# Performance work log

Hardware: AMD Instinct MI355X
Metric: run time of the kernel (lower is better)

The kernel has to match this reference:

```python
import jax, jax.numpy as jnp
import numpy as np

DEPTH = 3


def _outer(a, b):
    # batched tensor product of flattened tensor-algebra levels: (B, m) x (B, n) -> (B, m*n)
    return (a[:, :, None] * b[:, None, :]).reshape(a.shape[0], -1)


def _signature(X, depth):
    """Truncated path signature via Chen's identity (matches signatory.signature,
    basepoint=False). X: (B, T, C) -> (B, sum_k C^k)."""
    B, T, C = X.shape
    dX = X[:, 1:, :] - X[:, :-1, :]  # (B, T-1, C) increments

    def exp_levels(dx):
        # exp(dx) in truncated tensor algebra: level k = dx^{\otimes k} / k!
        e = [dx]
        for k in range(2, depth + 1):
            e.append(_outer(e[-1], dx) / k)
        return e

    def step(S, dx):
        e = exp_levels(dx)
        new = []
        for k in range(1, depth + 1):
            t = S[k - 1] + e[k - 1]  # terms with S_0=1 or e_0=1
            for i in range(1, k):
                t = t + _outer(S[i - 1], e[k - i - 1])
            new.append(t)
        return tuple(new), None

    init = tuple(jnp.zeros((B, C ** k), X.dtype) for k in range(1, depth + 1))
    S, _ = jax.lax.scan(step, init, jnp.swapaxes(dX, 0, 1))  # scan over time
    return jnp.concatenate(S, axis=1)


def setup_inputs() -> dict:
    key = jax.random.key(0)
    kx, kw, kb = jax.random.split(key, 3)
    B, T, C, n_out = 2048, 128, 8, 10
    sig_dim = sum(C ** k for k in range(1, DEPTH + 1))  # 584
    X = jax.random.normal(kx, (B, T, C), dtype=jnp.float32)
    bound = 1.0 / np.sqrt(sig_dim)
    W = jax.random.uniform(kw, (n_out, sig_dim), jnp.float32, -bound, bound)
    b = jax.random.uniform(kb, (n_out,), jnp.float32, -bound, bound)
    return {"X": X, "W": W, "b": b}


def reference(X, W, b):
    sig = _signature(X, DEPTH)          # (B, sig_dim)
    out = sig @ W.T + b                  # (B, n_outputs)
    return out.reshape(-1, W.shape[0])
```

## Files before the change

kernel.cpp:

```cpp
#include <hip/hip_runtime.h>

#define B_TOTAL 2048
#define T_LEN 128
#define C_DIM 8
#define NOUT 10
#define SIG_DIM 584
#define WAVES_PER_BLOCK 4

__global__ __launch_bounds__(256) void sig_linear_kernel(
    const float* __restrict__ X, const float* __restrict__ W,
    const float* __restrict__ bias, float* __restrict__ out)
{
    __shared__ __align__(16) float lds[WAVES_PER_BLOCK][T_LEN * C_DIM];
    const int tid = threadIdx.x;
    const int w = tid >> 6;
    const int l = tid & 63;
    const int b = blockIdx.x * WAVES_PER_BLOCK + w;
    const int i = l >> 3;
    const int j = l & 7;

    const float4* Xb4 = reinterpret_cast<const float4*>(X + (size_t)b * (T_LEN * C_DIM));
    float4* lds4 = reinterpret_cast<float4*>(&lds[w][0]);
#pragma unroll
    for (int r = 0; r < 4; ++r) lds4[r * 64 + l] = Xb4[r * 64 + l];
    __syncthreads();

    const float* L = &lds[w][0];

    float s3[8];
#pragma unroll
    for (int k = 0; k < 8; ++k) s3[k] = 0.f;
    float s2 = 0.f, s1i = 0.f, s1j = 0.f;

    float xp[8];
    {
        float4 r0 = *reinterpret_cast<const float4*>(L);
        float4 r1 = *reinterpret_cast<const float4*>(L + 4);
        xp[0] = r0.x; xp[1] = r0.y; xp[2] = r0.z; xp[3] = r0.w;
        xp[4] = r1.x; xp[5] = r1.y; xp[6] = r1.z; xp[7] = r1.w;
    }
    float xpi = L[i], xpj = L[j];

    for (int t = 1; t < T_LEN; ++t) {
        const float* row = L + t * C_DIM;
        float4 r0 = *reinterpret_cast<const float4*>(row);
        float4 r1 = *reinterpret_cast<const float4*>(row + 4);
        float xc[8];
        xc[0] = r0.x; xc[1] = r0.y; xc[2] = r0.z; xc[3] = r0.w;
        xc[4] = r1.x; xc[5] = r1.y; xc[6] = r1.z; xc[7] = r1.w;
        float xci = row[i], xcj = row[j];

        float dx[8];
#pragma unroll
        for (int k = 0; k < 8; ++k) { dx[k] = xc[k] - xp[k]; xp[k] = xc[k]; }
        float dxi = xci - xpi, dxj = xcj - xpj;
        xpi = xci; xpj = xcj;

        float cij = dxi * dxj;
        float f = s2 + 0.5f * s1i * dxj + (1.0f / 6.0f) * cij;
#pragma unroll
        for (int k = 0; k < 8; ++k) s3[k] = fmaf(f, dx[k], s3[k]);
        s2 = fmaf(0.5f, cij, fmaf(s1i, dxj, s2));
        s1i += dxi;
        s1j += dxj;
    }

#pragma unroll
    for (int o = 0; o < NOUT; ++o) {
        const float* wrow = W + o * SIG_DIM;
        float part = s2 * wrow[8 + l];
        const float4 w0 = *reinterpret_cast<const float4*>(wrow + 72 + l * 8);
        const float4 w1 = *reinterpret_cast<const float4*>(wrow + 72 + l * 8 + 4);
        part = fmaf(s3[0], w0.x, part); part = fmaf(s3[1], w0.y, part);
        part = fmaf(s3[2], w0.z, part); part = fmaf(s3[3], w0.w, part);
        part = fmaf(s3[4], w1.x, part); part = fmaf(s3[5], w1.y, part);
        part = fmaf(s3[6], w1.z, part); part = fmaf(s3[7], w1.w, part);
        if (i == 0) part = fmaf(s1j, wrow[j], part);
#pragma unroll
        for (int off = 32; off > 0; off >>= 1) part += __shfl_xor(part, off);
        if (l == 0) out[b * NOUT + o] = part + bias[o];
    }
}

extern "C" void kernel_launch(void* const* d_in, const int* in_sizes, int n_in,
                              void* d_out, int out_size, void* d_ws, size_t ws_size,
                              hipStream_t stream) {
    const float* X = (const float*)d_in[0];
    const float* W = (const float*)d_in[1];
    const float* bias = (const float*)d_in[2];
    float* out = (float*)d_out;
    dim3 grid(B_TOTAL / WAVES_PER_BLOCK);
    dim3 block(64 * WAVES_PER_BLOCK);
    sig_linear_kernel<<<grid, block, 0, stream>>>(X, W, bias, out);
}
```

Baseline: 23.57 us.

## Split each path's time scan across four waves and merge with Chen's identity

Assigns one batch element per block and splits its 127 time steps across four waves, each computing a partial signature over 32 increments. The partial signatures go to LDS and are combined sequentially with Chen's identity, and the output dot products are spread across waves. Increments are precomputed into LDS and broadcast with readlane instead of being recomputed by every lane. This shortens the serial dependency chain per wave and adds parallelism, at the cost of extra LDS traffic, barriers and merge arithmetic.

```diff
diff --git a/kernel.cpp b/kernel.cpp
--- a/kernel.cpp
+++ b/kernel.cpp
@@ -1,72 +1,119 @@
 #include <hip/hip_runtime.h>
 
-#define B_TOTAL 2048
-#define T_LEN 128
-#define C_DIM 8
 #define NOUT 10
 #define SIG_DIM 584
-#define WAVES_PER_BLOCK 4
 
-__global__ __launch_bounds__(256) void sig_linear_kernel(
+__device__ __forceinline__ float rdlane(float x, int lane) {
+    return __int_as_float(__builtin_amdgcn_readlane(__float_as_int(x), lane));
+}
+
+__global__ __launch_bounds__(256, 4) void sig_linear_kernel(
     const float* __restrict__ X, const float* __restrict__ W,
     const float* __restrict__ bias, float* __restrict__ out)
 {
-    __shared__ __align__(16) float lds[WAVES_PER_BLOCK][T_LEN * C_DIM];
+    __shared__ __align__(16) float s_path[1024];
+    __shared__ __align__(16) float s_dx[1024];
+    __shared__ __align__(16) float s_sig[4 * SIG_DIM];
+
     const int tid = threadIdx.x;
     const int w = tid >> 6;
     const int l = tid & 63;
-    const int b = blockIdx.x * WAVES_PER_BLOCK + w;
     const int i = l >> 3;
     const int j = l & 7;
+    const int b = blockIdx.x;
 
-    const float4* Xb4 = reinterpret_cast<const float4*>(X + (size_t)b * (T_LEN * C_DIM));
-    float4* lds4 = reinterpret_cast<float4*>(&lds[w][0]);
-#pragma unroll
-    for (int r = 0; r < 4; ++r) lds4[r * 64 + l] = Xb4[r * 64 + l];
+    const float4* Xb4 = reinterpret_cast<const float4*>(X + (size_t)b * 1024);
+    reinterpret_cast<float4*>(s_path)[tid] = Xb4[tid];
     __syncthreads();
 
-    const float* L = &lds[w][0];
+    const int idx = w * 256 + l * 4;
+    const bool v = idx < 1016;
+    float4 d4;
+    {
+        const float4 a  = *reinterpret_cast<const float4*>(s_path + idx);
+        const float4 c4 = *reinterpret_cast<const float4*>(s_path + (v ? idx + 8 : idx));
+        d4.x = v ? (c4.x - a.x) : 0.f;
+        d4.y = v ? (c4.y - a.y) : 0.f;
+        d4.z = v ? (c4.z - a.z) : 0.f;
+        d4.w = v ? (c4.w - a.w) : 0.f;
+        *reinterpret_cast<float4*>(s_dx + idx) = d4;
+    }
+    __syncthreads();
 
     float s3[8];
 #pragma unroll
     for (int k = 0; k < 8; ++k) s3[k] = 0.f;
     float s2 = 0.f, s1i = 0.f, s1j = 0.f;
 
-    float xp[8];
-    {
-        float4 r0 = *reinterpret_cast<const float4*>(L);
-        float4 r1 = *reinterpret_cast<const float4*>(L + 4);
-        xp[0] = r0.x; xp[1] = r0.y; xp[2] = r0.z; xp[3] = r0.w;
-        xp[4] = r1.x; xp[5] = r1.y; xp[6] = r1.z; xp[7] = r1.w;
-    }
-    float xpi = L[i], xpj = L[j];
-
-    for (int t = 1; t < T_LEN; ++t) {
-        const float* row = L + t * C_DIM;
-        float4 r0 = *reinterpret_cast<const float4*>(row);
-        float4 r1 = *reinterpret_cast<const float4*>(row + 4);
-        float xc[8];
-        xc[0] = r0.x; xc[1] = r0.y; xc[2] = r0.z; xc[3] = r0.w;
-        xc[4] = r1.x; xc[5] = r1.y; xc[6] = r1.z; xc[7] = r1.w;
-        float xci = row[i], xcj = row[j];
-
-        float dx[8];
+    const float* dxb = s_dx + w * 256;
 #pragma unroll
-        for (int k = 0; k < 8; ++k) { dx[k] = xc[k] - xp[k]; xp[k] = xc[k]; }
-        float dxi = xci - xpi, dxj = xcj - xpj;
-        xpi = xci; xpj = xcj;
-
-        float cij = dxi * dxj;
-        float f = s2 + 0.5f * s1i * dxj + (1.0f / 6.0f) * cij;
-#pragma unroll
-        for (int k = 0; k < 8; ++k) s3[k] = fmaf(f, dx[k], s3[k]);
-        s2 = fmaf(0.5f, cij, fmaf(s1i, dxj, s2));
+    for (int s = 0; s < 32; ++s) {
+        const float dxi = dxb[s * 8 + i];
+        const float dxj = dxb[s * 8 + j];
+        const float k0 = rdlane(d4.x, 2 * s);
+        const float k1 = rdlane(d4.y, 2 * s);
+        const float k2 = rdlane(d4.z, 2 * s);
+        const float k3 = rdlane(d4.w, 2 * s);
+        const float k4 = rdlane(d4.x, 2 * s + 1);
+        const float k5 = rdlane(d4.y, 2 * s + 1);
+        const float k6 = rdlane(d4.z, 2 * s + 1);
+        const float k7 = rdlane(d4.w, 2 * s + 1);
+        const float c = dxi * dxj;
+        const float u = s1i * dxj;
+        const float f = fmaf(0.5f, u, fmaf(1.0f / 6.0f, c, s2));
+        s3[0] = fmaf(f, k0, s3[0]);
+        s3[1] = fmaf(f, k1, s3[1]);
+        s3[2] = fmaf(f, k2, s3[2]);
+        s3[3] = fmaf(f, k3, s3[3]);
+        s3[4] = fmaf(f, k4, s3[4]);
+        s3[5] = fmaf(f, k5, s3[5]);
+        s3[6] = fmaf(f, k6, s3[6]);
+        s3[7] = fmaf(f, k7, s3[7]);
+        s2 = fmaf(0.5f, c, s2 + u);
         s1i += dxi;
         s1j += dxj;
     }
 
+    {
+        float* sg = s_sig + w * SIG_DIM;
+        if (i == 0) sg[j] = s1j;
+        sg[8 + l] = s2;
+        *reinterpret_cast<float4*>(sg + 72 + l * 8) =
+            make_float4(s3[0], s3[1], s3[2], s3[3]);
+        *reinterpret_cast<float4*>(sg + 72 + l * 8 + 4) =
+            make_float4(s3[4], s3[5], s3[6], s3[7]);
+    }
+    __syncthreads();
+
 #pragma unroll
-    for (int o = 0; o < NOUT; ++o) {
+    for (int k = 0; k < 8; ++k) s3[k] = 0.f;
+    s2 = 0.f; s1i = 0.f; s1j = 0.f;
+#pragma unroll
+    for (int c = 0; c < 4; ++c) {
+        const float* sg = s_sig + c * SIG_DIM;
+        const float4 b0 = *reinterpret_cast<const float4*>(sg);
+        const float4 b1 = *reinterpret_cast<const float4*>(sg + 4);
+        const float s1bi = sg[i];
+        const float s1bj = sg[j];
+        const float s2b = sg[8 + l];
+        const float4 q0 = *reinterpret_cast<const float4*>(sg + 8 + j * 8);
+        const float4 q1 = *reinterpret_cast<const float4*>(sg + 8 + j * 8 + 4);
+        const float4 t0 = *reinterpret_cast<const float4*>(sg + 72 + l * 8);
+        const float4 t1 = *reinterpret_cast<const float4*>(sg + 72 + l * 8 + 4);
+        s3[0] = fmaf(s2, b0.x, fmaf(s1i, q0.x, s3[0] + t0.x));
+        s3[1] = fmaf(s2, b0.y, fmaf(s1i, q0.y, s3[1] + t0.y));
+        s3[2] = fmaf(s2, b0.z, fmaf(s1i, q0.z, s3[2] + t0.z));
+        s3[3] = fmaf(s2, b0.w, fmaf(s1i, q0.w, s3[3] + t0.w));
+        s3[4] = fmaf(s2, b1.x, fmaf(s1i, q1.x, s3[4] + t1.x));
+        s3[5] = fmaf(s2, b1.y, fmaf(s1i, q1.y, s3[5] + t1.y));
+        s3[6] = fmaf(s2, b1.z, fmaf(s1i, q1.z, s3[6] + t1.z));
+        s3[7] = fmaf(s2, b1.w, fmaf(s1i, q1.w, s3[7] + t1.w));
+        s2 = s2 + fmaf(s1i, s1bj, s2b);
+        s1i += s1bi;
+        s1j += s1bj;
+    }
+
+    for (int o = w; o < NOUT; o += 4) {
         const float* wrow = W + o * SIG_DIM;
         float part = s2 * wrow[8 + l];
         const float4 w0 = *reinterpret_cast<const float4*>(wrow + 72 + l * 8);
@@ -89,7 +136,5 @@
     const float* W = (const float*)d_in[1];
     const float* bias = (const float*)d_in[2];
     float* out = (float*)d_out;
-    dim3 grid(B_TOTAL / WAVES_PER_BLOCK);
-    dim3 block(64 * WAVES_PER_BLOCK);
-    sig_linear_kernel<<<grid, block, 0, stream>>>(X, W, bias, out);
+    sig_linear_kernel<<<dim3(2048), dim3(256), 0, stream>>>(X, W, bias, out);
 }
```

Result: slower. 24.72 us (+4.9%).

## Precompute increments in transposed LDS and broadcast dx via readlane

Applied to the files above, without the earlier changes.

Each lane now computes path increments directly from global memory and stores them time-major per channel in padded LDS. In the time loop the full dx vector comes from scalar readlane broadcasts of register-held increments, and each lane's own i/j increments are read as float4 from the transposed columns. This removes the per-step subtraction and the repeated full-row LDS reads, at the cost of a fully unrolled 127-step loop with many readlane operations and more code.

```diff
diff --git a/kernel.cpp b/kernel.cpp
--- a/kernel.cpp
+++ b/kernel.cpp
@@ -1,69 +1,102 @@
 #include <hip/hip_runtime.h>
 
-#define B_TOTAL 2048
-#define T_LEN 128
-#define C_DIM 8
 #define NOUT 10
 #define SIG_DIM 584
-#define WAVES_PER_BLOCK 4
+#define TPAD 132
+
+__device__ __forceinline__ float rdlane(float x, int lane) {
+    return __int_as_float(__builtin_amdgcn_readlane(__float_as_int(x), lane));
+}
 
 __global__ __launch_bounds__(256) void sig_linear_kernel(
     const float* __restrict__ X, const float* __restrict__ W,
     const float* __restrict__ bias, float* __restrict__ out)
 {
-    __shared__ __align__(16) float lds[WAVES_PER_BLOCK][T_LEN * C_DIM];
+    __shared__ float s_dxT[4][8 * TPAD];
+
     const int tid = threadIdx.x;
     const int w = tid >> 6;
     const int l = tid & 63;
-    const int b = blockIdx.x * WAVES_PER_BLOCK + w;
     const int i = l >> 3;
     const int j = l & 7;
+    const int b = blockIdx.x * 4 + w;
 
-    const float4* Xb4 = reinterpret_cast<const float4*>(X + (size_t)b * (T_LEN * C_DIM));
-    float4* lds4 = reinterpret_cast<float4*>(&lds[w][0]);
-#pragma unroll
-    for (int r = 0; r < 4; ++r) lds4[r * 64 + l] = Xb4[r * 64 + l];
+    const float* Xb = X + (size_t)b * 1024;
+    float* dxT = &s_dxT[w][0];
+    const int cb = (l & 1) * 4;
+    const int rl = l >> 1;
+
+    float4 dA, dB, dC, dD;
+#define PREP(DQ, QQ)                                                          \
+    {                                                                         \
+        const int r = (QQ) * 32 + rl;                                         \
+        const float* xr = Xb + r * 8 + cb;                                    \
+        const float4 a  = *reinterpret_cast<const float4*>(xr);               \
+        const float4 c4 = *reinterpret_cast<const float4*>(xr + (r < 127 ? 8 : 0)); \
+        DQ.x = (r < 127) ? c4.x - a.x : 0.f;                                  \
+        DQ.y = (r < 127) ? c4.y - a.y : 0.f;                                  \
+        DQ.z = (r < 127) ? c4.z - a.z : 0.f;                                  \
+        DQ.w = (r < 127) ? c4.w - a.w : 0.f;                                  \
+        dxT[(cb + 0) * TPAD + r] = DQ.x;                                      \
+        dxT[(cb + 1) * TPAD + r] = DQ.y;                                      \
+        dxT[(cb + 2) * TPAD + r] = DQ.z;                                      \
+        dxT[(cb + 3) * TPAD + r] = DQ.w;                                      \
+    }
+    PREP(dA, 0) PREP(dB, 1) PREP(dC, 2) PREP(dD, 3)
+#undef PREP
     __syncthreads();
-
-    const float* L = &lds[w][0];
 
     float s3[8];
 #pragma unroll
     for (int k = 0; k < 8; ++k) s3[k] = 0.f;
     float s2 = 0.f, s1i = 0.f, s1j = 0.f;
 
-    float xp[8];
-    {
-        float4 r0 = *reinterpret_cast<const float4*>(L);
-        float4 r1 = *reinterpret_cast<const float4*>(L + 4);
-        xp[0] = r0.x; xp[1] = r0.y; xp[2] = r0.z; xp[3] = r0.w;
-        xp[4] = r1.x; xp[5] = r1.y; xp[6] = r1.z; xp[7] = r1.w;
+    const float* icol = dxT + i * TPAD;
+    const float* jcol = dxT + j * TPAD;
+
+#define STEP(DQ, LB, DXI, DXJ)                                                \
+    {                                                                         \
+        const float k0 = rdlane(DQ.x, (LB));                                  \
+        const float k1 = rdlane(DQ.y, (LB));                                  \
+        const float k2 = rdlane(DQ.z, (LB));                                  \
+        const float k3 = rdlane(DQ.w, (LB));                                  \
+        const float k4 = rdlane(DQ.x, (LB) + 1);                              \
+        const float k5 = rdlane(DQ.y, (LB) + 1);                              \
+        const float k6 = rdlane(DQ.z, (LB) + 1);                              \
+        const float k7 = rdlane(DQ.w, (LB) + 1);                              \
+        const float cc = (DXI) * (DXJ);                                       \
+        const float uu = s1i * (DXJ);                                         \
+        const float f  = fmaf(0.5f, uu, fmaf(1.0f / 6.0f, cc, s2));           \
+        s3[0] = fmaf(f, k0, s3[0]);                                           \
+        s3[1] = fmaf(f, k1, s3[1]);                                           \
+        s3[2] = fmaf(f, k2, s3[2]);                                           \
+        s3[3] = fmaf(f, k3, s3[3]);                                           \
+        s3[4] = fmaf(f, k4, s3[4]);                                           \
+        s3[5] = fmaf(f, k5, s3[5]);                                           \
+        s3[6] = fmaf(f, k6, s3[6]);                                           \
+        s3[7] = fmaf(f, k7, s3[7]);                                           \
+        s2 = fmaf(0.5f, cc, s2 + uu);                                         \
+        s1i += (DXI);                                                         \
+        s1j += (DXJ);                                                         \
     }
-    float xpi = L[i], xpj = L[j];
 
-    for (int t = 1; t < T_LEN; ++t) {
-        const float* row = L + t * C_DIM;
-        float4 r0 = *reinterpret_cast<const float4*>(row);
-        float4 r1 = *reinterpret_cast<const float4*>(row + 4);
-        float xc[8];
-        xc[0] = r0.x; xc[1] = r0.y; xc[2] = r0.z; xc[3] = r0.w;
-        xc[4] = r1.x; xc[5] = r1.y; xc[6] = r1.z; xc[7] = r1.w;
-        float xci = row[i], xcj = row[j];
-
-        float dx[8];
-#pragma unroll
-        for (int k = 0; k < 8; ++k) { dx[k] = xc[k] - xp[k]; xp[k] = xc[k]; }
-        float dxi = xci - xpi, dxj = xcj - xpj;
-        xpi = xci; xpj = xcj;
-
-        float cij = dxi * dxj;
-        float f = s2 + 0.5f * s1i * dxj + (1.0f / 6.0f) * cij;
-#pragma unroll
-        for (int k = 0; k < 8; ++k) s3[k] = fmaf(f, dx[k], s3[k]);
-        s2 = fmaf(0.5f, cij, fmaf(s1i, dxj, s2));
-        s1i += dxi;
-        s1j += dxj;
+#define SECTION(DQ, QQ)                                                       \
+    for (int g = 0; g < 8; ++g) {                                             \
+        const int t0 = (QQ) * 32 + g * 4;                                     \
+        const float4 ic = *reinterpret_cast<const float4*>(icol + t0);        \
+        const float4 jc = *reinterpret_cast<const float4*>(jcol + t0);        \
+        const int lb = g * 8;                                                 \
+        STEP(DQ, lb + 0, ic.x, jc.x)                                          \
+        STEP(DQ, lb + 2, ic.y, jc.y)                                          \
+        STEP(DQ, lb + 4, ic.z, jc.z)                                          \
+        STEP(DQ, lb + 6, ic.w, jc.w)                                          \
     }
+    SECTION(dA, 0)
+    SECTION(dB, 1)
+    SECTION(dC, 2)
+    SECTION(dD, 3)
+#undef SECTION
+#undef STEP
 
 #pragma unroll
     for (int o = 0; o < NOUT; ++o) {
@@ -89,7 +122,5 @@
     const float* W = (const float*)d_in[1];
     const float* bias = (const float*)d_in[2];
     float* out = (float*)d_out;
-    dim3 grid(B_TOTAL / WAVES_PER_BLOCK);
-    dim3 block(64 * WAVES_PER_BLOCK);
-    sig_linear_kernel<<<grid, block, 0, stream>>>(X, W, bias, out);
+    sig_linear_kernel<<<dim3(512), dim3(256), 0, stream>>>(X, W, bias, out);
 }
```

Result: faster. 21.60 us (-8.4%).

## Split each path's time scan across four waves using algebraic level-3 decomposition

Applied to the files above, without the earlier changes.

Instead of one wave scanning all 127 steps for one batch element, each block now handles one element and each of its four waves covers a 32-step time chunk. The level-3 signature is rewritten algebraically so that chunks add independently: the S2 sums are combined through LDS and the X_T term is applied once in the epilogue. Per-step row broadcasts use readlane from registers instead of LDS reads, and a transposed LDS layout serves the i/j columns. This shortens the serial dependency chain by about four times, at the cost of more blocks, extra syncs and a cross-wave reduction of partial outputs.

```diff
diff --git a/kernel.cpp b/kernel.cpp
--- a/kernel.cpp
+++ b/kernel.cpp
@@ -1,85 +1,144 @@
 #include <hip/hip_runtime.h>
 
-#define B_TOTAL 2048
-#define T_LEN 128
-#define C_DIM 8
 #define NOUT 10
 #define SIG_DIM 584
-#define WAVES_PER_BLOCK 4
+#define TS 36
+
+__device__ __forceinline__ float rdlane(float x, int lane) {
+    return __int_as_float(__builtin_amdgcn_readlane(__float_as_int(x), lane));
+}
+__device__ __forceinline__ float comp4(float4 v, int c) {
+    return c == 0 ? v.x : c == 1 ? v.y : c == 2 ? v.z : v.w;
+}
 
 __global__ __launch_bounds__(256) void sig_linear_kernel(
     const float* __restrict__ X, const float* __restrict__ W,
     const float* __restrict__ bias, float* __restrict__ out)
 {
-    __shared__ __align__(16) float lds[WAVES_PER_BLOCK][T_LEN * C_DIM];
+    __shared__ __align__(16) float s_xT[4][8 * TS];
+    __shared__ float s_s2[4][64];
+    __shared__ float s_part[4][16];
+
     const int tid = threadIdx.x;
-    const int w = tid >> 6;
-    const int l = tid & 63;
-    const int b = blockIdx.x * WAVES_PER_BLOCK + w;
-    const int i = l >> 3;
-    const int j = l & 7;
+    const int w = tid >> 6, l = tid & 63, i = l >> 3, j = l & 7;
+    const int b = blockIdx.x;
+    const int t0 = w * 32;
+    const float* Xb = X + (size_t)b * 1024;
 
-    const float4* Xb4 = reinterpret_cast<const float4*>(X + (size_t)b * (T_LEN * C_DIM));
-    float4* lds4 = reinterpret_cast<float4*>(&lds[w][0]);
-#pragma unroll
-    for (int r = 0; r < 4; ++r) lds4[r * 64 + l] = Xb4[r * 64 + l];
+    const int rl_ = l >> 1, cb = (l & 1) * 4;
+    const float4 d4 = *reinterpret_cast<const float4*>(Xb + (t0 + rl_) * 8 + cb);
+    float* xT = &s_xT[w][0];
+    xT[(cb + 0) * TS + rl_] = d4.x;
+    xT[(cb + 1) * TS + rl_] = d4.y;
+    xT[(cb + 2) * TS + rl_] = d4.z;
+    xT[(cb + 3) * TS + rl_] = d4.w;
+    if (l < 2) {
+        const int rN = (t0 + 32 < 128) ? t0 + 32 : 127;
+        const float4 e4 = *reinterpret_cast<const float4*>(Xb + rN * 8 + l * 4);
+        xT[(l * 4 + 0) * TS + 32] = e4.x;
+        xT[(l * 4 + 1) * TS + 32] = e4.y;
+        xT[(l * 4 + 2) * TS + 32] = e4.z;
+        xT[(l * 4 + 3) * TS + 32] = e4.w;
+    }
+    const float x0i = Xb[i];
+    const float x0j = Xb[j];
+    const float s1jv = Xb[1016 + j] - x0j;
     __syncthreads();
 
-    const float* L = &lds[w][0];
+    float A[8];
+#pragma unroll
+    for (int k = 0; k < 8; ++k) A[k] = 0.f;
+    float S2f = 0.f;
 
-    float s3[8];
+    const float* icol = xT + i * TS;
+    const float* jcol = xT + j * TS;
+
+    float xcr[8], xnr[8];
 #pragma unroll
-    for (int k = 0; k < 8; ++k) s3[k] = 0.f;
-    float s2 = 0.f, s1i = 0.f, s1j = 0.f;
+    for (int k = 0; k < 8; ++k)
+        xcr[k] = rdlane(comp4(d4, k & 3), k >> 2);
 
-    float xp[8];
-    {
-        float4 r0 = *reinterpret_cast<const float4*>(L);
-        float4 r1 = *reinterpret_cast<const float4*>(L + 4);
-        xp[0] = r0.x; xp[1] = r0.y; xp[2] = r0.z; xp[3] = r0.w;
-        xp[4] = r1.x; xp[5] = r1.y; xp[6] = r1.z; xp[7] = r1.w;
-    }
-    float xpi = L[i], xpj = L[j];
+    float4 ic = *reinterpret_cast<const float4*>(icol);
+    float4 jc = *reinterpret_cast<const float4*>(jcol);
 
-    for (int t = 1; t < T_LEN; ++t) {
-        const float* row = L + t * C_DIM;
-        float4 r0 = *reinterpret_cast<const float4*>(row);
-        float4 r1 = *reinterpret_cast<const float4*>(row + 4);
-        float xc[8];
-        xc[0] = r0.x; xc[1] = r0.y; xc[2] = r0.z; xc[3] = r0.w;
-        xc[4] = r1.x; xc[5] = r1.y; xc[6] = r1.z; xc[7] = r1.w;
-        float xci = row[i], xcj = row[j];
-
-        float dx[8];
 #pragma unroll
-        for (int k = 0; k < 8; ++k) { dx[k] = xc[k] - xp[k]; xp[k] = xc[k]; }
-        float dxi = xci - xpi, dxj = xcj - xpj;
-        xpi = xci; xpj = xcj;
-
-        float cij = dxi * dxj;
-        float f = s2 + 0.5f * s1i * dxj + (1.0f / 6.0f) * cij;
+    for (int g4 = 0; g4 < 8; ++g4) {
+        float4 in4, jn4;
+        if (g4 < 7) {
+            in4 = *reinterpret_cast<const float4*>(icol + 4 * g4 + 4);
+            jn4 = *reinterpret_cast<const float4*>(jcol + 4 * g4 + 4);
+        } else {
+            in4 = make_float4(icol[32], 0.f, 0.f, 0.f);
+            jn4 = make_float4(jcol[32], 0.f, 0.f, 0.f);
+        }
 #pragma unroll
-        for (int k = 0; k < 8; ++k) s3[k] = fmaf(f, dx[k], s3[k]);
-        s2 = fmaf(0.5f, cij, fmaf(s1i, dxj, s2));
-        s1i += dxi;
-        s1j += dxj;
+        for (int q = 0; q < 4; ++q) {
+            const int s = g4 * 4 + q;
+            const float xci = comp4(ic, q);
+            const float xcj = comp4(jc, q);
+            const float xni = (q < 3) ? comp4(ic, q + 1) : in4.x;
+            const float xnj = (q < 3) ? comp4(jc, q + 1) : jn4.x;
+            if (s < 31) {
+#pragma unroll
+                for (int k = 0; k < 8; ++k)
+                    xnr[k] = rdlane(comp4(d4, k & 3), 2 * (s + 1) + (k >> 2));
+            } else {
+#pragma unroll
+                for (int k = 0; k < 8; ++k) xnr[k] = xT[k * TS + 32];
+            }
+            const float dxi = xni - xci;
+            const float dxj = xnj - xcj;
+            const float cpi = xci - x0i;
+            const float cpj = xcj - x0j;
+            (void)cpj;
+            const float gg = dxj * fmaf(0.5f, dxi, cpi);
+            const float hh = dxj * fmaf(1.0f / 6.0f, dxi, 0.5f * cpi);
+            const float gmh = gg - hh;
+            S2f += gg;
+#pragma unroll
+            for (int k = 0; k < 8; ++k)
+                A[k] = fmaf(gmh, xnr[k], fmaf(hh, xcr[k], A[k]));
+#pragma unroll
+            for (int k = 0; k < 8; ++k) xcr[k] = xnr[k];
+        }
+        ic = in4;
+        jc = jn4;
     }
 
+    s_s2[w][l] = S2f;
+    __syncthreads();
+    const float S2T = s_s2[0][l] + s_s2[1][l] + s_s2[2][l] + s_s2[3][l];
+
+    const float4 x7a = *reinterpret_cast<const float4*>(Xb + 1016);
+    const float4 x7b = *reinterpret_cast<const float4*>(Xb + 1020);
 #pragma unroll
     for (int o = 0; o < NOUT; ++o) {
         const float* wrow = W + o * SIG_DIM;
-        float part = s2 * wrow[8 + l];
         const float4 w0 = *reinterpret_cast<const float4*>(wrow + 72 + l * 8);
         const float4 w1 = *reinterpret_cast<const float4*>(wrow + 72 + l * 8 + 4);
-        part = fmaf(s3[0], w0.x, part); part = fmaf(s3[1], w0.y, part);
-        part = fmaf(s3[2], w0.z, part); part = fmaf(s3[3], w0.w, part);
-        part = fmaf(s3[4], w1.x, part); part = fmaf(s3[5], w1.y, part);
-        part = fmaf(s3[6], w1.z, part); part = fmaf(s3[7], w1.w, part);
-        if (i == 0) part = fmaf(s1j, wrow[j], part);
+        float dA = w0.x * A[0];
+        dA = fmaf(w0.y, A[1], dA); dA = fmaf(w0.z, A[2], dA);
+        dA = fmaf(w0.w, A[3], dA); dA = fmaf(w1.x, A[4], dA);
+        dA = fmaf(w1.y, A[5], dA); dA = fmaf(w1.z, A[6], dA);
+        dA = fmaf(w1.w, A[7], dA);
+        float part = -dA;
+        if (w == 0) {
+            float e = w0.x * x7a.x;
+            e = fmaf(w0.y, x7a.y, e); e = fmaf(w0.z, x7a.z, e);
+            e = fmaf(w0.w, x7a.w, e); e = fmaf(w1.x, x7b.x, e);
+            e = fmaf(w1.y, x7b.y, e); e = fmaf(w1.z, x7b.z, e);
+            e = fmaf(w1.w, x7b.w, e);
+            part = fmaf(S2T, e + wrow[8 + l], part);
+            if (i == 0) part = fmaf(s1jv, wrow[j], part);
+        }
 #pragma unroll
         for (int off = 32; off > 0; off >>= 1) part += __shfl_xor(part, off);
-        if (l == 0) out[b * NOUT + o] = part + bias[o];
+        if (l == o) s_part[w][o] = part;
     }
+    __syncthreads();
+    if (tid < NOUT)
+        out[b * NOUT + tid] = s_part[0][tid] + s_part[1][tid] +
+                              s_part[2][tid] + s_part[3][tid] + bias[tid];
 }
 
 extern "C" void kernel_launch(void* const* d_in, const int* in_sizes, int n_in,
@@ -89,7 +148,5 @@
     const float* W = (const float*)d_in[1];
     const float* bias = (const float*)d_in[2];
     float* out = (float*)d_out;
-    dim3 grid(B_TOTAL / WAVES_PER_BLOCK);
-    dim3 block(64 * WAVES_PER_BLOCK);
-    sig_linear_kernel<<<grid, block, 0, stream>>>(X, W, bias, out);
+    sig_linear_kernel<<<dim3(2048), dim3(256), 0, stream>>>(X, W, bias, out);
 }
```

After: 26.69 us. 1.13x slower.
